# Performance work log

Measured on AMD Instinct MI355X. Metric: run time of the kernel, lower is better.

The kernel has to match this reference:

```python
import jax, jax.numpy as jnp
import numpy as np

EPS = 1e-6
BETA = 0.5
B, T, N = 128, 30, 10000   # batch, BP iterations, n error bits
M, K = 5000, 10            # checks, observables
CHK_W, OBS_W = 6, 50       # row weights of chkmat / obsmat


def _make_supports():
    """Deterministic sparse supports (CSR-style flattened col indices + row ids)."""
    rng = np.random.default_rng(0)
    chk_rows = np.argpartition(rng.random((M, N)), CHK_W, axis=1)[:, :CHK_W]
    obs_rows = np.argpartition(rng.random((K, N)), OBS_W, axis=1)[:, :OBS_W]
    chk_idx = chk_rows.reshape(-1).astype(np.int32)
    chk_seg = np.repeat(np.arange(M, dtype=np.int32), CHK_W)
    obs_idx = obs_rows.reshape(-1).astype(np.int32)
    obs_seg = np.repeat(np.arange(K, dtype=np.int32), OBS_W)
    return chk_idx, chk_seg, obs_idx, obs_seg


def setup_inputs() -> dict:
    key = jax.random.key(0)
    k1, k2, k3 = jax.random.split(key, 3)
    all_llrs = jax.random.normal(k1, (B, T, N), dtype=jnp.float32) * 2.0
    syndromes = jax.random.randint(k2, (B, M), 0, 2, dtype=jnp.int32)
    observables = jax.random.randint(k3, (B, K), 0, 2, dtype=jnp.int32)
    chk_idx, chk_seg, obs_idx, obs_seg = _make_supports()
    return {
        "all_llrs": all_llrs,
        "syndromes": syndromes,
        "observables": observables,
        "chk_idx": jnp.asarray(chk_idx),
        "chk_seg": jnp.asarray(chk_seg),
        "obs_idx": jnp.asarray(obs_idx),
        "obs_seg": jnp.asarray(obs_seg),
    }


def _pred_llr(t, idx, seg, num_seg):
    # t: (B,T,N) tanh(llr/2); gather support cols -> (B,T,E)
    g = t[:, :, idx]
    # segmented product over support entries (tanh rule), segments on axis 0
    p = jax.ops.segment_prod(jnp.moveaxis(g, 2, 0), seg, num_segments=num_seg)  # (S,B,T)
    p = jnp.clip(jnp.moveaxis(p, 0, 2), -1.0 + EPS, 1.0 - EPS)  # (B,T,S)
    return 2.0 * jnp.arctanh(p)


def _bce_with_logits(z, y):
    # stable BCEWithLogits: max(z,0) - z*y + log(1+exp(-|z|)) == logaddexp(0,z) - z*y
    return jnp.logaddexp(0.0, z) - z * y


def reference(all_llrs, syndromes, observables, chk_idx, chk_seg, obs_idx, obs_seg):
    t = jnp.tanh(all_llrs * 0.5)                                   # (B,T,N)
    syn_llr = _pred_llr(t, chk_idx, chk_seg, syndromes.shape[1])    # (B,T,M)
    obs_llr = _pred_llr(t, obs_idx, obs_seg, observables.shape[1])  # (B,T,K)
    y_syn = syndromes.astype(jnp.float32)[:, None, :]
    y_obs = observables.astype(jnp.float32)[:, None, :]
    loss1 = _bce_with_logits(-syn_llr, y_syn).sum(axis=2)           # (B,T)
    loss2 = _bce_with_logits(-obs_llr, y_obs).sum(axis=2)           # (B,T)
    loss = BETA * loss1 + (1.0 - BETA) * loss2
    return loss.mean()
```

## Files before the change

kernel.cpp:

```cpp
#include <hip/hip_runtime.h>

typedef float floatx2 __attribute__((ext_vector_type(2)));

#define B_  128
#define T_  30
#define N_  10000
#define M_  5000
#define K_  10
#define OBS_W_ 50
#define EPS_ 1e-6f
#define LOG2F_ 0.69314718056f
#define BT_  3840
#define CHUNK_ 40
#define SEGW_  (CHUNK_ / 4)
#define NCHK_ (M_/CHUNK_)
#define NB_ 10

__device__ __forceinline__ float tanh_half(float x) {
    float r = __builtin_amdgcn_rcpf(__expf(x) + 1.f);
    return __builtin_fmaf(-2.f, r, 1.f);
}

__global__ __launch_bounds__(256) void tanh_transpose_fp8(
    const float*   __restrict__ llrs,
    unsigned char* __restrict__ tt)
{
    __shared__ unsigned int lds[64][65];
    const int bt0 = blockIdx.x * 256;
    const int n0  = blockIdx.y * 64;
    const int tid = threadIdx.x;
    const int c4  = tid & 15;
    const int r4b = tid >> 4;

    #pragma unroll
    for (int it = 0; it < 4; ++it) {
        const int r4 = r4b + 16 * it;
        if (n0 + 4 * c4 < N_) {
            float t[4][4];
            #pragma unroll
            for (int j = 0; j < 4; ++j) {
                float4 v = *(const float4*)(llrs +
                            (size_t)(bt0 + 4 * r4 + j) * N_ + n0 + 4 * c4);
                t[j][0] = tanh_half(v.x);
                t[j][1] = tanh_half(v.y);
                t[j][2] = tanh_half(v.z);
                t[j][3] = tanh_half(v.w);
            }
            #pragma unroll
            for (int k = 0; k < 4; ++k) {
                int pk = __builtin_amdgcn_cvt_pk_fp8_f32(t[0][k], t[1][k], 0, false);
                pk     = __builtin_amdgcn_cvt_pk_fp8_f32(t[2][k], t[3][k], pk, true);
                lds[r4][4 * c4 + k] = (unsigned int)pk;
            }
        }
    }
    __syncthreads();

    const int w = tid & 15;
    #pragma unroll
    for (int it = 0; it < 4; ++it) {
        const int col = (tid >> 4) + 16 * it;
        if (n0 + col < N_) {
            uint4 d;
            d.x = lds[4 * w + 0][col];
            d.y = lds[4 * w + 1][col];
            d.z = lds[4 * w + 2][col];
            d.w = lds[4 * w + 3][col];
            *(uint4*)(tt + (size_t)(n0 + col) * BT_ + bt0 + 16 * w) = d;
        }
    }
}

__device__ __forceinline__ void cvt4(unsigned int qv, float* a) {
    floatx2 lo = __builtin_amdgcn_cvt_pk_f32_fp8((int)qv, false);
    floatx2 hi = __builtin_amdgcn_cvt_pk_f32_fp8((int)qv, true);
    a[0] = lo.x; a[1] = lo.y; a[2] = hi.x; a[3] = hi.y;
}

__global__ __launch_bounds__(256) void gather_loss_fp8(
    const unsigned char* __restrict__ tt,
    const int*           __restrict__ syndromes,
    const int*           __restrict__ observables,
    const int*           __restrict__ chk_idx,
    const int*           __restrict__ obs_idx,
    float*               __restrict__ out)
{
    __shared__ int   sidx[CHUNK_ * 6];
    __shared__ int   ssyn[NB_][CHUNK_];
    __shared__ float red[4];

    const int tid  = threadIdx.x;
    const int lane = tid & 63;
    const int wave = tid >> 6;
    const int r0   = blockIdx.x * 256 + lane * 4;
    const int bA   = r0 / 30;
    const int bB   = (r0 + 3) / 30;
    const int split= (bA + 1) * 30 - r0;
    const int b_lo = (blockIdx.x * 256) / 30;
    const unsigned char* col0 = tt + r0;
    const int y = blockIdx.y;
    float acc = 0.f;

    if (y < NCHK_) {
        const int m0 = y * CHUNK_;
        for (int i = tid; i < CHUNK_ * 6; i += 256)
            sidx[i] = chk_idx[m0 * 6 + i];
        for (int i = tid; i < NB_ * CHUNK_; i += 256) {
            int bi = i / CHUNK_, j = i - bi * CHUNK_;
            int b  = b_lo + bi; if (b > B_ - 1) b = B_ - 1;
            ((int*)ssyn)[i] = syndromes[(size_t)b * M_ + m0 + j];
        }
        __syncthreads();
        const int iA = bA - b_lo, iB = bB - b_lo;

        #pragma unroll 2
        for (int s = wave * SEGW_; s < wave * SEGW_ + SEGW_; ++s) {
            int i0 = sidx[s * 6 + 0], i1 = sidx[s * 6 + 1], i2 = sidx[s * 6 + 2];
            int i3 = sidx[s * 6 + 3], i4 = sidx[s * 6 + 4], i5 = sidx[s * 6 + 5];
            unsigned int q0 = *(const unsigned int*)(col0 + (size_t)i0 * BT_);
            unsigned int q1 = *(const unsigned int*)(col0 + (size_t)i1 * BT_);
            unsigned int q2 = *(const unsigned int*)(col0 + (size_t)i2 * BT_);
            unsigned int q3 = *(const unsigned int*)(col0 + (size_t)i3 * BT_);
            unsigned int q4 = *(const unsigned int*)(col0 + (size_t)i4 * BT_);
            unsigned int q5 = *(const unsigned int*)(col0 + (size_t)i5 * BT_);
            float a[4], b4[4], p[4];
            cvt4(q0, p);  cvt4(q1, a);  cvt4(q2, b4);
            #pragma unroll
            for (int j = 0; j < 4; ++j) p[j] *= a[j] * b4[j];
            cvt4(q3, a);  cvt4(q4, b4);
            #pragma unroll
            for (int j = 0; j < 4; ++j) p[j] *= a[j] * b4[j];
            cvt4(q5, a);
            float sgA = ssyn[iA][s] ? -1.f : 1.f;
            float sgB = ssyn[iB][s] ? -1.f : 1.f;
            #pragma unroll
            for (int j = 0; j < 4; ++j) {
                float sg = (j >= split) ? sgB : sgA;
                float sp = sg * p[j] * a[j];
                sp = fminf(fmaxf(sp, -1.f + EPS_), 1.f - EPS_);
                acc += 1.0f - __log2f(1.f + sp);
            }
        }
    } else {
        for (int k = wave; k < K_; k += 4) {
            const int* oi = obs_idx + k * OBS_W_;
            float p[4] = {1.f, 1.f, 1.f, 1.f};
            #pragma unroll 5
            for (int j2 = 0; j2 < OBS_W_; ++j2) {
                unsigned int qq = *(const unsigned int*)(col0 + (size_t)oi[j2] * BT_);
                float a[4];
                cvt4(qq, a);
                p[0] *= a[0]; p[1] *= a[1]; p[2] *= a[2]; p[3] *= a[3];
            }
            float sgA = observables[(size_t)bA * K_ + k] ? -1.f : 1.f;
            float sgB = observables[(size_t)bB * K_ + k] ? -1.f : 1.f;
            #pragma unroll
            for (int j = 0; j < 4; ++j) {
                float sg = (j >= split) ? sgB : sgA;
                float sp = sg * p[j];
                sp = fminf(fmaxf(sp, -1.f + EPS_), 1.f - EPS_);
                acc += 1.0f - __log2f(1.f + sp);
            }
        }
    }

    #pragma unroll
    for (int off = 32; off > 0; off >>= 1)
        acc += __shfl_down(acc, off, 64);
    if (lane == 0) red[wave] = acc;
    __syncthreads();
    if (tid == 0) {
        float s = red[0] + red[1] + red[2] + red[3];
        atomicAdd(out, s * (0.5f * LOG2F_ / (float)BT_));
    }
}

extern "C" void kernel_launch(void* const* d_in, const int* in_sizes, int n_in,
                              void* d_out, int out_size, void* d_ws, size_t ws_size,
                              hipStream_t stream) {
    const float* all_llrs    = (const float*)d_in[0];
    const int*   syndromes   = (const int*)d_in[1];
    const int*   observables = (const int*)d_in[2];
    const int*   chk_idx     = (const int*)d_in[3];
    const int*   obs_idx     = (const int*)d_in[5];
    float*         out = (float*)d_out;
    unsigned char* tt  = (unsigned char*)d_ws;

    hipMemsetAsync(out, 0, sizeof(float) * out_size, stream);

    dim3 g1(BT_ / 256, (N_ + 63) / 64);
    tanh_transpose_fp8<<<g1, 256, 0, stream>>>(all_llrs, tt);

    dim3 g2(BT_ / 256, NCHK_ + 1);
    gather_loss_fp8<<<g2, 256, 0, stream>>>(
        tt, syndromes, observables, chk_idx, obs_idx, out);
}
```

Before: 284.8 us.

## Drop memset and atomics via last-block reduction; enlarge check chunks with prefetched gathers

Removes the hipMemsetAsync launch and the per-block atomicAdd on the output. Each block now writes its partial sum to workspace, and the last block to finish (found through an agent-scope counter reset by the first kernel) reduces the partials and writes the result. The check chunk grows from 40 to 100 so fewer blocks are launched. The gather loop is software-pipelined with double-buffered registers, issuing the next segment's six loads before consuming the current ones. The cost is more registers per thread and fewer blocks to spread across the CUs.

```diff
diff --git a/kernel.cpp b/kernel.cpp
--- a/kernel.cpp
+++ b/kernel.cpp
@@ -11,10 +11,14 @@
 #define EPS_ 1e-6f
 #define LOG2F_ 0.69314718056f
 #define BT_  3840
-#define CHUNK_ 40
+#define CHUNK_ 100
 #define SEGW_  (CHUNK_ / 4)
 #define NCHK_ (M_/CHUNK_)
 #define NB_ 10
+#define GX_ (BT_ / 256)
+#define NBLK_ ((NCHK_ + 1) * GX_)
+#define PART_OFF_ (40u * 1024u * 1024u)
+#define CNT_OFF_  (PART_OFF_ + 65536u)
 
 __device__ __forceinline__ float tanh_half(float x) {
     float r = __builtin_amdgcn_rcpf(__expf(x) + 1.f);
@@ -23,8 +27,12 @@
 
 __global__ __launch_bounds__(256) void tanh_transpose_fp8(
     const float*   __restrict__ llrs,
-    unsigned char* __restrict__ tt)
+    unsigned char* __restrict__ tt,
+    unsigned int*  __restrict__ donecnt)
 {
+    if (blockIdx.x == 0 && blockIdx.y == 0 && threadIdx.x == 0)
+        *donecnt = 0u;
+
     __shared__ unsigned int lds[64][65];
     const int bt0 = blockIdx.x * 256;
     const int n0  = blockIdx.y * 64;
@@ -77,17 +85,52 @@
     a[0] = lo.x; a[1] = lo.y; a[2] = hi.x; a[3] = hi.y;
 }
 
+__device__ __forceinline__ void issue6(const int* __restrict__ sidx, int s,
+                                       const unsigned char* __restrict__ col0,
+                                       unsigned int* q) {
+    #pragma unroll
+    for (int t = 0; t < 6; ++t) {
+        int it = sidx[s * 6 + t];
+        q[t] = *(const unsigned int*)(col0 + (size_t)it * BT_);
+    }
+}
+
+__device__ __forceinline__ float consume6(const unsigned int* q,
+                                          float sgA, float sgB, int split) {
+    float a[4], b4[4], p[4];
+    cvt4(q[0], p);  cvt4(q[1], a);  cvt4(q[2], b4);
+    #pragma unroll
+    for (int j = 0; j < 4; ++j) p[j] *= a[j] * b4[j];
+    cvt4(q[3], a);  cvt4(q[4], b4);
+    #pragma unroll
+    for (int j = 0; j < 4; ++j) p[j] *= a[j] * b4[j];
+    cvt4(q[5], a);
+    float local = 0.f;
+    #pragma unroll
+    for (int j = 0; j < 4; ++j) {
+        float sg = (j >= split) ? sgB : sgA;
+        float sp = sg * p[j] * a[j];
+        sp = fminf(fmaxf(sp, -1.f + EPS_), 1.f - EPS_);
+        local += 1.0f - __log2f(1.f + sp);
+    }
+    return local;
+}
+
 __global__ __launch_bounds__(256) void gather_loss_fp8(
     const unsigned char* __restrict__ tt,
     const int*           __restrict__ syndromes,
     const int*           __restrict__ observables,
     const int*           __restrict__ chk_idx,
     const int*           __restrict__ obs_idx,
-    float*               __restrict__ out)
+    float*               __restrict__ partials,
+    unsigned int*        __restrict__ donecnt,
+    float*               __restrict__ out,
+    int                  out_size)
 {
     __shared__ int   sidx[CHUNK_ * 6];
     __shared__ int   ssyn[NB_][CHUNK_];
     __shared__ float red[4];
+    __shared__ int   lastFlag;
 
     const int tid  = threadIdx.x;
     const int lane = tid & 63;
@@ -112,34 +155,17 @@
         }
         __syncthreads();
         const int iA = bA - b_lo, iB = bB - b_lo;
-
-        #pragma unroll 2
-        for (int s = wave * SEGW_; s < wave * SEGW_ + SEGW_; ++s) {
-            int i0 = sidx[s * 6 + 0], i1 = sidx[s * 6 + 1], i2 = sidx[s * 6 + 2];
-            int i3 = sidx[s * 6 + 3], i4 = sidx[s * 6 + 4], i5 = sidx[s * 6 + 5];
-            unsigned int q0 = *(const unsigned int*)(col0 + (size_t)i0 * BT_);
-            unsigned int q1 = *(const unsigned int*)(col0 + (size_t)i1 * BT_);
-            unsigned int q2 = *(const unsigned int*)(col0 + (size_t)i2 * BT_);
-            unsigned int q3 = *(const unsigned int*)(col0 + (size_t)i3 * BT_);
-            unsigned int q4 = *(const unsigned int*)(col0 + (size_t)i4 * BT_);
-            unsigned int q5 = *(const unsigned int*)(col0 + (size_t)i5 * BT_);
-            float a[4], b4[4], p[4];
-            cvt4(q0, p);  cvt4(q1, a);  cvt4(q2, b4);
-            #pragma unroll
-            for (int j = 0; j < 4; ++j) p[j] *= a[j] * b4[j];
-            cvt4(q3, a);  cvt4(q4, b4);
-            #pragma unroll
-            for (int j = 0; j < 4; ++j) p[j] *= a[j] * b4[j];
-            cvt4(q5, a);
+        const int sBeg = wave * SEGW_;
+
+        unsigned int q[2][6];
+        issue6(sidx, sBeg, col0, q[0]);
+        #pragma unroll
+        for (int k = 0; k < SEGW_; ++k) {
+            const int s = sBeg + k;
+            if (k + 1 < SEGW_) issue6(sidx, s + 1, col0, q[(k + 1) & 1]);
             float sgA = ssyn[iA][s] ? -1.f : 1.f;
             float sgB = ssyn[iB][s] ? -1.f : 1.f;
-            #pragma unroll
-            for (int j = 0; j < 4; ++j) {
-                float sg = (j >= split) ? sgB : sgA;
-                float sp = sg * p[j] * a[j];
-                sp = fminf(fmaxf(sp, -1.f + EPS_), 1.f - EPS_);
-                acc += 1.0f - __log2f(1.f + sp);
-            }
+            acc += consume6(q[k & 1], sgA, sgB, split);
         }
     } else {
         for (int k = wave; k < K_; k += 4) {
@@ -169,9 +195,31 @@
         acc += __shfl_down(acc, off, 64);
     if (lane == 0) red[wave] = acc;
     __syncthreads();
+
     if (tid == 0) {
-        float s = red[0] + red[1] + red[2] + red[3];
-        atomicAdd(out, s * (0.5f * LOG2F_ / (float)BT_));
+        float bsum = red[0] + red[1] + red[2] + red[3];
+        const int slot = y * GX_ + blockIdx.x;
+        __hip_atomic_store(&partials[slot], bsum,
+                           __ATOMIC_RELEASE, __HIP_MEMORY_SCOPE_AGENT);
+        unsigned prev = __hip_atomic_fetch_add(donecnt, 1u,
+                           __ATOMIC_ACQ_REL, __HIP_MEMORY_SCOPE_AGENT);
+        lastFlag = (prev == NBLK_ - 1);
+    }
+    __syncthreads();
+    if (lastFlag) {
+        float s = 0.f;
+        for (int i = tid; i < NBLK_; i += 256)
+            s += __hip_atomic_load(&partials[i],
+                                   __ATOMIC_ACQUIRE, __HIP_MEMORY_SCOPE_AGENT);
+        #pragma unroll
+        for (int off = 32; off > 0; off >>= 1)
+            s += __shfl_down(s, off, 64);
+        if (lane == 0) red[wave] = s;
+        __syncthreads();
+        if (tid == 0)
+            out[0] = (red[0] + red[1] + red[2] + red[3])
+                     * (0.5f * LOG2F_ / (float)BT_);
+        for (int i = tid + 1; i < out_size; i += 256) out[i] = 0.f;
     }
 }
 
@@ -185,13 +233,14 @@
     const int*   obs_idx     = (const int*)d_in[5];
     float*         out = (float*)d_out;
     unsigned char* tt  = (unsigned char*)d_ws;
-
-    hipMemsetAsync(out, 0, sizeof(float) * out_size, stream);
-
-    dim3 g1(BT_ / 256, (N_ + 63) / 64);
-    tanh_transpose_fp8<<<g1, 256, 0, stream>>>(all_llrs, tt);
-
-    dim3 g2(BT_ / 256, NCHK_ + 1);
+    float*        partials = (float*)((unsigned char*)d_ws + PART_OFF_);
+    unsigned int* donecnt  = (unsigned int*)((unsigned char*)d_ws + CNT_OFF_);
+
+    dim3 g1(GX_, (N_ + 63) / 64);
+    tanh_transpose_fp8<<<g1, 256, 0, stream>>>(all_llrs, tt, donecnt);
+
+    dim3 g2(GX_, NCHK_ + 1);
     gather_loss_fp8<<<g2, 256, 0, stream>>>(
-        tt, syndromes, observables, chk_idx, obs_idx, out);
-}
+        tt, syndromes, observables, chk_idx, obs_idx,
+        partials, donecnt, out, out_size);
+}
```

Result: slower. 296.1 us (+4.0%).
